# Kernel optimization log

Hardware: AMD Instinct MI355X
Metric: run time of the kernel (lower is better)

Reference implementation:

```python
import jax, jax.numpy as jnp
import numpy as np

VOCAB = 50257
DIM = 768
DROPOUT = 0.1


def setup_inputs() -> dict:
    key = jax.random.key(0)
    k_w, k_m, k_i = jax.random.split(key, 3)
    weight = jax.random.normal(k_w, (VOCAB, DIM), dtype=jnp.float32)
    # Row-wise bernoulli dropout mask, pre-scaled by 1/(1-p), exactly as
    # dropout_mask() in the torch source: bernoulli_(1 - p) / (1 - p)
    keep = jax.random.bernoulli(k_m, 1.0 - DROPOUT, (VOCAB, 1))
    mask = keep.astype(jnp.float32) / jnp.float32(1.0 - DROPOUT)
    words = jax.random.randint(k_i, (8, 2048), 0, VOCAB, dtype=jnp.int32)
    return {"words": words, "weight": weight, "mask": mask}


def reference(words, weight, mask):
    # training path: mask full (V, D) table row-wise, then gather rows.
    # padding_idx is None -> -1 sentinel -> no padding behavior; scale is None.
    masked_weight = weight * mask  # (V, D), broadcast over D
    return jnp.take(masked_weight, words, axis=0)  # (B, S, D)
```

## Files before the change

### kernel.cpp

```cpp
#include <hip/hip_runtime.h>


#define DIM 768
#define VEC4_PER_ROW (DIM / 4)

__global__ __launch_bounds__(VEC4_PER_ROW) void embed_dropout_kernel(
    const int* __restrict__ words,
    const float* __restrict__ weight,
    const float* __restrict__ mask,
    float* __restrict__ out) {
    const int token = blockIdx.x;
    const int idx = words[token];
    const float scale = mask[idx];

    const float4* __restrict__ wrow =
        (const float4*)(weight + (size_t)idx * DIM);
    float4* __restrict__ orow = (float4*)(out + (size_t)token * DIM);

    const int t = threadIdx.x;
    float4 v = wrow[t];
    v.x *= scale;
    v.y *= scale;
    v.z *= scale;
    v.w *= scale;
    orow[t] = v;
}

extern "C" void kernel_launch(void* const* d_in, const int* in_sizes, int n_in,
                              void* d_out, int out_size, void* d_ws, size_t ws_size,
                              hipStream_t stream) {
    const int* words = (const int*)d_in[0];
    const float* weight = (const float*)d_in[1];
    const float* mask = (const float*)d_in[2];
    float* out = (float*)d_out;

    const int n_tokens = in_sizes[0];

    embed_dropout_kernel<<<n_tokens, VEC4_PER_ROW, 0, stream>>>(
        words, weight, mask, out);
}
```

Baseline: 211.6 us.

## Flatten gather into grid-stride float4 work with 8 loads in flight and nontemporal stores

Replaces the one-block-per-token launch (192 threads) with 256-thread blocks that each handle 8 strided float4 elements over the flattened output. All loads are issued before any computation, which raises memory-level parallelism, and the output is written with nontemporal stores so it does not pollute the cache. The cost is extra integer division per element to recover token and offset, plus redundant words and mask lookups.

```diff
diff --git a/kernel.cpp b/kernel.cpp
--- a/kernel.cpp
+++ b/kernel.cpp
@@ -2,28 +2,51 @@
 
 
 #define DIM 768
-#define VEC4_PER_ROW (DIM / 4)
+#define V4_PER_ROW (DIM / 4)
+#define ELEMS 8
+#define BLOCK 256
 
-__global__ __launch_bounds__(VEC4_PER_ROW) void embed_dropout_kernel(
+typedef float f4 __attribute__((ext_vector_type(4)));
+
+__global__ __launch_bounds__(BLOCK) void embed_dropout_kernel(
     const int* __restrict__ words,
     const float* __restrict__ weight,
     const float* __restrict__ mask,
-    float* __restrict__ out) {
-    const int token = blockIdx.x;
-    const int idx = words[token];
-    const float scale = mask[idx];
+    f4* __restrict__ out,
+    unsigned int total4) {
+    const unsigned int base =
+        blockIdx.x * (BLOCK * ELEMS) + threadIdx.x;
 
-    const float4* __restrict__ wrow =
-        (const float4*)(weight + (size_t)idx * DIM);
-    float4* __restrict__ orow = (float4*)(out + (size_t)token * DIM);
+    unsigned int ii[ELEMS];
+    unsigned int tok[ELEMS];
+    unsigned int r[ELEMS];
+    int idx[ELEMS];
 
-    const int t = threadIdx.x;
-    float4 v = wrow[t];
-    v.x *= scale;
-    v.y *= scale;
-    v.z *= scale;
-    v.w *= scale;
-    orow[t] = v;
+    #pragma unroll
+    for (int k = 0; k < ELEMS; ++k) {
+        unsigned int i = base + (unsigned int)k * BLOCK;
+        if (i >= total4) i = total4 - 1;
+        ii[k] = i;
+        tok[k] = i / V4_PER_ROW;
+        r[k] = i - tok[k] * V4_PER_ROW;
+        idx[k] = words[tok[k]];
+    }
+
+    float scale[ELEMS];
+    f4 v[ELEMS];
+    #pragma unroll
+    for (int k = 0; k < ELEMS; ++k) {
+        scale[k] = mask[idx[k]];
+        const f4* wrow =
+            (const f4*)(weight + (size_t)idx[k] * DIM) + r[k];
+        v[k] = *wrow;
+    }
+
+    #pragma unroll
+    for (int k = 0; k < ELEMS; ++k) {
+        f4 o = v[k] * scale[k];
+        __builtin_nontemporal_store(o, &out[ii[k]]);
+    }
 }
 
 extern "C" void kernel_launch(void* const* d_in, const int* in_sizes, int n_in,
@@ -32,10 +55,12 @@
     const int* words = (const int*)d_in[0];
     const float* weight = (const float*)d_in[1];
     const float* mask = (const float*)d_in[2];
-    float* out = (float*)d_out;
+    f4* out = (f4*)d_out;
 
-    const int n_tokens = in_sizes[0];
+    const unsigned int total4 = (unsigned int)(out_size / 4);
+    const unsigned int per_block = BLOCK * ELEMS;
+    const unsigned int grid = (total4 + per_block - 1) / per_block;
 
-    embed_dropout_kernel<<<n_tokens, VEC4_PER_ROW, 0, stream>>>(
-        words, weight, mask, out);
+    embed_dropout_kernel<<<grid, BLOCK, 0, stream>>>(
+        words, weight, mask, out, total4);
 }
```

Result: no change. 215.2 us (+1.7%).
